# Kernel optimization log

Measured on AMD Instinct MI355X. Metric: run time of the kernel, lower is better.

## Reference

```python
import jax, jax.numpy as jnp
import numpy as np

S, B, H = 512, 64, 1024


def setup_inputs() -> dict:
    key = jax.random.key(0)
    ks = jax.random.split(key, 9)
    sc = 1.0 / np.sqrt(2 * H)
    return {
        "hidden": jax.random.normal(ks[0], (B, H), jnp.float32),
        "decoder_out": jax.random.normal(ks[1], (B, H), jnp.float32),
        "encoder_states": jax.random.normal(ks[2], (S, B, H), jnp.float32),
        "W_attn": jax.random.uniform(ks[3], (2 * H, 2 * H), jnp.float32, -sc, sc),
        "b_attn": jax.random.uniform(ks[4], (2 * H,), jnp.float32, -sc, sc),
        "W_attn2": jax.random.uniform(ks[5], (1, 2 * H), jnp.float32, -sc, sc),
        "b_attn2": jax.random.uniform(ks[6], (1,), jnp.float32, -sc, sc),
        "W_comb": jax.random.uniform(ks[7], (H, 2 * H), jnp.float32, -sc, sc),
        "b_comb": jax.random.uniform(ks[8], (H,), jnp.float32, -sc, sc),
    }


def reference(hidden, decoder_out, encoder_states, W_attn, b_attn, W_attn2, b_attn2, W_comb, b_comb):
    s, b, h = encoder_states.shape
    # per-timestep cat(hidden, enc_t) -> attn -> tanh -> attn2, fully batched over S
    hid = jnp.broadcast_to(hidden[None], (s, b, h))
    cat = jnp.concatenate([hid, encoder_states], axis=-1)            # [S,B,2H]
    scores = jnp.tanh(cat @ W_attn.T + b_attn) @ W_attn2.T + b_attn2  # [S,B,1]
    scores = scores[..., 0].T                                         # [B,S] (stack dim=1 + squeeze)
    attn_w = jax.nn.softmax(scores, axis=-1)                          # [B,S]
    # bmm([B,1,S], [B,S,H]) -> [B,H]
    applied = jnp.einsum("bs,sbh->bh", attn_w, encoder_states)
    out = jnp.concatenate([decoder_out, applied], axis=-1) @ W_comb.T + b_comb
    out = jnp.tanh(out)
    return out, applied
```

## Files before the change

### kernel.cpp

```cpp
#include <hip/hip_runtime.h>
#include <stdint.h>


typedef __attribute__((ext_vector_type(8))) short bf16x8;
typedef __attribute__((ext_vector_type(4))) float f32x4;

__device__ __forceinline__ float bf2f(uint16_t u) {
  return __uint_as_float(((uint32_t)u) << 16);
}
__device__ __forceinline__ uint16_t f2bf(float x) {
  uint32_t u = __float_as_uint(x);
  u += 0x7fffu + ((u >> 16) & 1u);
  return (uint16_t)(u >> 16);
}
__device__ __forceinline__ uint32_t pk2(float a, float b) {
  return (uint32_t)f2bf(a) | ((uint32_t)f2bf(b) << 16);
}
__device__ __forceinline__ uint4 cvt8(const float* __restrict__ p) {
  const float4 a = *(const float4*)p;
  const float4 b = *(const float4*)(p + 4);
  uint4 r;
  r.x = pk2(a.x, a.y); r.y = pk2(a.z, a.w);
  r.z = pk2(b.x, b.y); r.w = pk2(b.z, b.w);
  return r;
}
__device__ __forceinline__ float tanh_fast(float x) {
  const float e = __expf(2.f * x);
  return __builtin_fmaf(-2.f, __builtin_amdgcn_rcpf(e + 1.f), 1.f);
}
__device__ __forceinline__ void load16(const uint16_t* g, uint16_t* l) {
  __builtin_amdgcn_global_load_lds(
      (const __attribute__((address_space(1))) void*)g,
      (__attribute__((address_space(3))) void*)l, 16, 0, 0);
}

__global__ __launch_bounds__(256)
void cvt_all_kernel(const float* __restrict__ enc, const float* __restrict__ Wa,
                    const float* __restrict__ Wc,
                    uint16_t* __restrict__ enc_bf, uint16_t* __restrict__ Wa_bf,
                    uint16_t* __restrict__ Wc_bf,
                    float* __restrict__ scores, float* __restrict__ U,
                    const float* __restrict__ ba) {
  const int tid0 = blockIdx.x * 256 + threadIdx.x;
  if (tid0 < 32768) {
    scores[tid0] = 0.f;
#pragma unroll
    for (int k = 0; k < 4; ++k) {
      const int i = tid0 * 4 + k;
      U[i] = ba[i & 2047];
    }
  }
  const int stride = gridDim.x * 256;
  for (int idx = tid0; idx < 4718592; idx += stride) {
    if (idx < 4194304) {
      ((uint4*)enc_bf)[idx] = cvt8(enc + (size_t)idx * 8);
    } else if (idx < 4456448) {
      const int k = idx - 4194304;
      const int j = k >> 7, c8 = k & 127;
      ((uint4*)Wa_bf)[k] = cvt8(Wa + (size_t)j * 2048 + 1024 + c8 * 8);
    } else {
      const int k = idx - 4456448;
      ((uint4*)Wc_bf)[k] = cvt8(Wc + (size_t)k * 8);
    }
  }
}

__global__ __launch_bounds__(256)
void gemm_u_kernel(const float* __restrict__ A, const float* __restrict__ B32,
                   float* __restrict__ U) {
  __shared__ __align__(16) uint16_t sA[128 * 32];
  __shared__ __align__(16) uint16_t sB[128 * 32];
  const int t = threadIdx.x, lane = t & 63, wave = t >> 6;
  const int wm = wave >> 1, wn = wave & 1;
  const int bn0 = blockIdx.x * 128;
  const int kbase = blockIdx.y * 256;
  const int srow = t >> 2, scol = (t & 3) * 8;
  const int ar0 = min(srow, 63), ar1 = min(64 + srow, 63);
  f32x4 acc[4][4];
#pragma unroll
  for (int i = 0; i < 4; ++i)
#pragma unroll
    for (int j = 0; j < 4; ++j) acc[i][j] = (f32x4){0.f, 0.f, 0.f, 0.f};
  const int mrow = wm * 64 + (lane & 15);
  const int nrow = wn * 64 + (lane & 15);
  const int kq = (lane >> 4) * 8;
  for (int kk = 0; kk < 8; ++kk) {
    const int k0 = kbase + (kk << 5);
    const uint4 va0 = cvt8(A + (size_t)ar0 * 1024 + scol + k0);
    const uint4 va1 = cvt8(A + (size_t)ar1 * 1024 + scol + k0);
    const uint4 vb0 = cvt8(B32 + (size_t)(bn0 + srow) * 2048 + scol + k0);
    const uint4 vb1 = cvt8(B32 + (size_t)(bn0 + 64 + srow) * 2048 + scol + k0);
    __syncthreads();
    *(uint4*)&sA[t * 8] = va0;
    *(uint4*)&sA[2048 + t * 8] = va1;
    *(uint4*)&sB[t * 8] = vb0;
    *(uint4*)&sB[2048 + t * 8] = vb1;
    __syncthreads();
    bf16x8 af[4], bfr[4];
#pragma unroll
    for (int i = 0; i < 4; ++i) af[i] = *(const bf16x8*)&sA[(mrow + i * 16) * 32 + kq];
#pragma unroll
    for (int j = 0; j < 4; ++j) bfr[j] = *(const bf16x8*)&sB[(nrow + j * 16) * 32 + kq];
#pragma unroll
    for (int i = 0; i < 4; ++i)
#pragma unroll
      for (int j = 0; j < 4; ++j)
        acc[i][j] = __builtin_amdgcn_mfma_f32_16x16x32_bf16(af[i], bfr[j], acc[i][j], 0, 0, 0);
  }
  const int colb = lane & 15, rquad = lane >> 4;
#pragma unroll
  for (int i = 0; i < 4; ++i)
#pragma unroll
    for (int r = 0; r < 4; ++r) {
      const int gm = wm * 64 + i * 16 + rquad * 4 + r;
      if (gm < 64) {
#pragma unroll
        for (int j = 0; j < 4; ++j) {
          const int gn = bn0 + wn * 64 + j * 16 + colb;
          atomicAdd(&U[gm * 2048 + gn], acc[i][j][r]);
        }
      }
    }
}

__global__ __launch_bounds__(512, 2)
void gemm_score_kernel(const uint16_t* __restrict__ A,
                       const uint16_t* __restrict__ Bm,
                       float* __restrict__ outf,
                       const float* __restrict__ Ubias,
                       const float* __restrict__ bias) {
  __shared__ __align__(16) uint16_t lds[3][2][8192];

  const int t = threadIdx.x, lane = t & 63, wave = t >> 6;
  const int wm = wave >> 2, wn = wave & 3;
  const int wid = blockIdx.x;
  const int xcd = wid & 7, q = wid >> 3;
  const int bm0 = (xcd * 16 + (q >> 3)) * 256;
  const int bn0 = (q & 7) * 256;

  const uint16_t* gpA[2];
  const uint16_t* gpB[2];
  int sb[2];
#pragma unroll
  for (int qq = 0; qq < 2; ++qq) {
    const int s = qq * 512 + t;
    const int r = s >> 2, kc = s & 3;
    const int g = kc ^ ((r >> 1) & 3);
    gpA[qq] = A + (size_t)(bm0 + r) * 1024 + g * 8;
    gpB[qq] = Bm + (size_t)(bn0 + r) * 1024 + g * 8;
    sb[qq] = (qq * 512 + wave * 64) * 8;
  }

  f32x4 acc[8][4];
#pragma unroll
  for (int i = 0; i < 8; ++i)
#pragma unroll
    for (int j = 0; j < 4; ++j) acc[i][j] = (f32x4){0.f, 0.f, 0.f, 0.f};

  const int swz = ((lane >> 1) & 3) << 3;
  const int kq = ((lane >> 4) * 8) ^ swz;
  const int aoff = (wm * 128 + (lane & 15)) * 32 + kq;
  const int boff = (wn * 64 + (lane & 15)) * 32 + kq;

#pragma unroll
  for (int qq = 0; qq < 2; ++qq) {
    load16(gpA[qq], &lds[0][0][sb[qq]]);
    load16(gpB[qq], &lds[0][1][sb[qq]]);
  }
#pragma unroll
  for (int qq = 0; qq < 2; ++qq) {
    load16(gpA[qq] + 32, &lds[1][0][sb[qq]]);
    load16(gpB[qq] + 32, &lds[1][1][sb[qq]]);
  }
  asm volatile("s_waitcnt vmcnt(4)" ::: "memory");
  __builtin_amdgcn_s_barrier();

  constexpr int NT = 32;
#pragma unroll
  for (int kt = 0; kt < NT; ++kt) {
    const int bufc = kt % 3;
    if (kt + 2 < NT) {
      const int nb = (kt + 2) % 3;
      const int kpre = (kt + 2) * 32;
#pragma unroll
      for (int qq = 0; qq < 2; ++qq) {
        load16(gpA[qq] + kpre, &lds[nb][0][sb[qq]]);
        load16(gpB[qq] + kpre, &lds[nb][1][sb[qq]]);
      }
    }
    const uint16_t* sA = lds[bufc][0];
    const uint16_t* sB = lds[bufc][1];
    bf16x8 af[8], bfr[4];
#pragma unroll
    for (int i = 0; i < 8; ++i) af[i] = *(const bf16x8*)&sA[aoff + i * 512];
#pragma unroll
    for (int j = 0; j < 4; ++j) bfr[j] = *(const bf16x8*)&sB[boff + j * 512];
#pragma unroll
    for (int i = 0; i < 8; ++i)
#pragma unroll
      for (int j = 0; j < 4; ++j)
        acc[i][j] = __builtin_amdgcn_mfma_f32_16x16x32_bf16(af[i], bfr[j], acc[i][j], 0, 0, 0);
    if (kt + 2 < NT) {
      asm volatile("s_waitcnt vmcnt(4) lgkmcnt(0)" ::: "memory");
      __builtin_amdgcn_s_barrier();
    } else if (kt + 1 < NT) {
      asm volatile("s_waitcnt vmcnt(0) lgkmcnt(0)" ::: "memory");
      __builtin_amdgcn_s_barrier();
    }
  }

  const int colb = lane & 15, rquad = lane >> 4;
  float w2f[4];
#pragma unroll
  for (int j = 0; j < 4; ++j) w2f[j] = bias[bn0 + wn * 64 + j * 16 + colb];
#pragma unroll
  for (int i = 0; i < 8; ++i) {
#pragma unroll
    for (int r = 0; r < 4; ++r) {
      const int gm = bm0 + wm * 128 + i * 16 + rquad * 4 + r;
      const int bb = gm & 63;
      float p = 0.f;
#pragma unroll
      for (int j = 0; j < 4; ++j) {
        const float u = Ubias[bb * 2048 + bn0 + wn * 64 + j * 16 + colb];
        p += tanh_fast(acc[i][j][r] + u) * w2f[j];
      }
      p += __shfl_xor(p, 1);
      p += __shfl_xor(p, 2);
      p += __shfl_xor(p, 4);
      p += __shfl_xor(p, 8);
      if (colb == 0) atomicAdd(outf + gm, p);
    }
  }
}

template <int NT>
__global__ __launch_bounds__(256)
void gemm_comb_kernel(const uint16_t* __restrict__ A, int lda,
                      const uint16_t* __restrict__ Bm, int ldb,
                      int M, float* __restrict__ outf,
                      const float* __restrict__ bias) {
  __shared__ __align__(16) uint16_t lds[3][2][4096];

  const int t = threadIdx.x, lane = t & 63, wave = t >> 6;
  const int wm = wave >> 1, wn = wave & 1;
  const int bm0 = 0;
  const int bn0 = blockIdx.y * 128;
  const int kbase = blockIdx.z * (NT * 32);

  const uint16_t* gpA[2];
  const uint16_t* gpB[2];
  int sb[2];
#pragma unroll
  for (int q = 0; q < 2; ++q) {
    const int s = q * 256 + t;
    const int r = s >> 2, kc = s & 3;
    const int g = kc ^ ((r >> 1) & 3);
    gpA[q] = A + (size_t)min(bm0 + r, M - 1) * lda + kbase + g * 8;
    gpB[q] = Bm + (size_t)(bn0 + r) * ldb + kbase + g * 8;
    sb[q] = (q * 256 + wave * 64) * 8;
  }

  f32x4 acc[4][4];
#pragma unroll
  for (int i = 0; i < 4; ++i)
#pragma unroll
    for (int j = 0; j < 4; ++j) acc[i][j] = (f32x4){0.f, 0.f, 0.f, 0.f};

  const int swz = ((lane >> 1) & 3) << 3;
  const int kq = ((lane >> 4) * 8) ^ swz;
  const int aoff = (wm * 64 + (lane & 15)) * 32 + kq;
  const int boff = (wn * 64 + (lane & 15)) * 32 + kq;

#pragma unroll
  for (int q = 0; q < 2; ++q) {
    load16(gpA[q], &lds[0][0][sb[q]]);
    load16(gpB[q], &lds[0][1][sb[q]]);
  }
#pragma unroll
  for (int q = 0; q < 2; ++q) {
    load16(gpA[q] + 32, &lds[1][0][sb[q]]);
    load16(gpB[q] + 32, &lds[1][1][sb[q]]);
  }
  asm volatile("s_waitcnt vmcnt(4)" ::: "memory");
  __builtin_amdgcn_s_barrier();

#pragma unroll
  for (int kt = 0; kt < NT; ++kt) {
    const int bufc = kt % 3;
    if (kt + 2 < NT) {
      const int nb = (kt + 2) % 3;
      const int kpre = (kt + 2) * 32;
#pragma unroll
      for (int q = 0; q < 2; ++q) {
        load16(gpA[q] + kpre, &lds[nb][0][sb[q]]);
        load16(gpB[q] + kpre, &lds[nb][1][sb[q]]);
      }
    }
    const uint16_t* sA = lds[bufc][0];
    const uint16_t* sB = lds[bufc][1];
    bf16x8 af[4], bfr[4];
#pragma unroll
    for (int i = 0; i < 4; ++i) af[i] = *(const bf16x8*)&sA[aoff + i * 512];
#pragma unroll
    for (int j = 0; j < 4; ++j) bfr[j] = *(const bf16x8*)&sB[boff + j * 512];
#pragma unroll
    for (int i = 0; i < 4; ++i)
#pragma unroll
      for (int j = 0; j < 4; ++j)
        acc[i][j] = __builtin_amdgcn_mfma_f32_16x16x32_bf16(af[i], bfr[j], acc[i][j], 0, 0, 0);
    if (kt + 2 < NT) {
      asm volatile("s_waitcnt vmcnt(4) lgkmcnt(0)" ::: "memory");
      __builtin_amdgcn_s_barrier();
    } else if (kt + 1 < NT) {
      asm volatile("s_waitcnt vmcnt(0) lgkmcnt(0)" ::: "memory");
      __builtin_amdgcn_s_barrier();
    }
  }

  const int colb = lane & 15, rquad = lane >> 4;
  const float bsc = (blockIdx.z == 0) ? 1.f : 0.f;
#pragma unroll
  for (int i = 0; i < 4; ++i)
#pragma unroll
    for (int r = 0; r < 4; ++r) {
      const int gm = bm0 + wm * 64 + i * 16 + rquad * 4 + r;
      if (gm < M) {
#pragma unroll
        for (int j = 0; j < 4; ++j) {
          const int gn = bn0 + wn * 64 + j * 16 + colb;
          atomicAdd(outf + gm * 1024 + gn, acc[i][j][r] + bsc * bias[gn]);
        }
      }
    }
}

__global__ __launch_bounds__(256)
void applied_kernel(const uint16_t* __restrict__ encb, const float* __restrict__ dec,
                    const float* __restrict__ scores,
                    float* __restrict__ out_applied, uint16_t* __restrict__ acat,
                    float* __restrict__ out_acc) {
  const int b = blockIdx.x, chunk = blockIdx.y, t = threadIdx.x;
  const int wave = t >> 6, lane = t & 63;
  __shared__ float w[512];
  __shared__ float red[8];
  __shared__ float2 part2[256];
  float v0 = scores[(size_t)t * 64 + b];
  float v1 = scores[(size_t)(t + 256) * 64 + b];
  float mx = fmaxf(v0, v1);
#pragma unroll
  for (int off = 32; off >= 1; off >>= 1) mx = fmaxf(mx, __shfl_xor(mx, off));
  if (lane == 0) red[wave] = mx;
  __syncthreads();
  mx = fmaxf(fmaxf(red[0], red[1]), fmaxf(red[2], red[3]));
  const float e0 = __expf(v0 - mx), e1 = __expf(v1 - mx);
  float sum = e0 + e1;
#pragma unroll
  for (int off = 32; off >= 1; off >>= 1) sum += __shfl_xor(sum, off);
  if (lane == 0) red[4 + wave] = sum;
  __syncthreads();
  sum = (red[4] + red[5]) + (red[6] + red[7]);
  const float inv = 1.f / sum;
  w[t] = e0 * inv;
  w[t + 256] = e1 * inv;
  __syncthreads();
  const int hp = t & 31, sq = t >> 5;
  const int h = chunk * 64 + hp * 2;
  const uint32_t* base = (const uint32_t*)encb + (size_t)b * 512 + (h >> 1);
  float a0 = 0.f, a1 = 0.f;
#pragma unroll 8
  for (int s = sq * 64; s < sq * 64 + 64; ++s) {
    const uint32_t p = base[(size_t)s * 32768];
    a0 += w[s] * bf2f((uint16_t)(p & 0xffffu));
    a1 += w[s] * bf2f((uint16_t)(p >> 16));
  }
  part2[t] = make_float2(a0, a1);
  __syncthreads();
  if (t < 32) {
    a0 = 0.f; a1 = 0.f;
#pragma unroll
    for (int k = 0; k < 8; ++k) {
      const float2 pp = part2[t + 32 * k];
      a0 += pp.x; a1 += pp.y;
    }
    *(float2*)(out_applied + (size_t)b * 1024 + h) = make_float2(a0, a1);
    *(uint32_t*)(acat + (size_t)b * 2048 + 1024 + h) = pk2(a0, a1);
    *(uint32_t*)(acat + (size_t)b * 2048 + h) =
        pk2(dec[(size_t)b * 1024 + h], dec[(size_t)b * 1024 + h + 1]);
    *(float2*)(out_acc + (size_t)b * 1024 + h) = make_float2(0.f, 0.f);
  }
}

__global__ __launch_bounds__(256)
void tanh_kernel(const float* __restrict__ acc, float* __restrict__ outp) {
  const int i = blockIdx.x * 256 + threadIdx.x;
  float4 v = ((const float4*)acc)[i];
  v.x = tanh_fast(v.x); v.y = tanh_fast(v.y);
  v.z = tanh_fast(v.z); v.w = tanh_fast(v.w);
  ((float4*)outp)[i] = v;
}

extern "C" void kernel_launch(void* const* d_in, const int* in_sizes, int n_in,
                              void* d_out, int out_size, void* d_ws, size_t ws_size,
                              hipStream_t stream) {
  const float* hidden  = (const float*)d_in[0];
  const float* dec     = (const float*)d_in[1];
  const float* enc     = (const float*)d_in[2];
  const float* W_attn  = (const float*)d_in[3];
  const float* b_attn  = (const float*)d_in[4];
  const float* W_attn2 = (const float*)d_in[5];
  const float* W_comb  = (const float*)d_in[7];
  const float* b_comb  = (const float*)d_in[8];
  float* outp = (float*)d_out;

  char* ws = (char*)d_ws;
  float*    scores = (float*)(ws + 0);
  float*    U      = (float*)(ws + 131072);
  float*    out_acc= (float*)(ws + 131072);
  uint16_t* acat   = (uint16_t*)(ws + 655360);
  uint16_t* enc_bf = (uint16_t*)(ws + 1048576);
  uint16_t* Wa_bf  = (uint16_t*)(ws + 68157440);
  uint16_t* Wc_bf  = (uint16_t*)(ws + 72351744);

  cvt_all_kernel<<<4608, 256, 0, stream>>>(enc, W_attn, W_comb, enc_bf, Wa_bf,
                                           Wc_bf, scores, U, b_attn);
  gemm_u_kernel<<<dim3(16, 4), 256, 0, stream>>>(hidden, W_attn, U);
  gemm_score_kernel<<<1024, 512, 0, stream>>>(enc_bf, Wa_bf, scores, U, W_attn2);
  applied_kernel<<<dim3(64, 16), 256, 0, stream>>>(enc_bf, dec, scores,
                                                   outp + 65536, acat, out_acc);
  gemm_comb_kernel<16><<<dim3(1, 8, 4), 256, 0, stream>>>(
      acat, 2048, Wc_bf, 2048, 64, out_acc, b_comb);
  tanh_kernel<<<64, 256, 0, stream>>>(out_acc, outp);
}
```

Before: 451.8 us.

## Switch score GEMM to double-buffered K=64 tiles with 8-way XOR swizzle

```diff
diff --git a/kernel.cpp b/kernel.cpp
--- a/kernel.cpp
+++ b/kernel.cpp
@@ -129,7 +129,7 @@
                        float* __restrict__ outf,
                        const float* __restrict__ Ubias,
                        const float* __restrict__ bias) {
-  __shared__ __align__(16) uint16_t lds[3][2][8192];
+  __shared__ __align__(16) uint16_t lds[2][2][16384];
 
   const int t = threadIdx.x, lane = t & 63, wave = t >> 6;
   const int wm = wave >> 2, wn = wave & 3;
@@ -138,14 +138,14 @@
   const int bm0 = (xcd * 16 + (q >> 3)) * 256;
   const int bn0 = (q & 7) * 256;
 
-  const uint16_t* gpA[2];
-  const uint16_t* gpB[2];
-  int sb[2];
-#pragma unroll
-  for (int qq = 0; qq < 2; ++qq) {
+  const uint16_t* gpA[4];
+  const uint16_t* gpB[4];
+  int sb[4];
+#pragma unroll
+  for (int qq = 0; qq < 4; ++qq) {
     const int s = qq * 512 + t;
-    const int r = s >> 2, kc = s & 3;
-    const int g = kc ^ ((r >> 1) & 3);
+    const int r = s >> 3, kc = s & 7;
+    const int g = kc ^ (r & 7);
     gpA[qq] = A + (size_t)(bm0 + r) * 1024 + g * 8;
     gpB[qq] = Bm + (size_t)(bn0 + r) * 1024 + g * 8;
     sb[qq] = (qq * 512 + wave * 64) * 8;
@@ -157,54 +157,61 @@
 #pragma unroll
     for (int j = 0; j < 4; ++j) acc[i][j] = (f32x4){0.f, 0.f, 0.f, 0.f};
 
-  const int swz = ((lane >> 1) & 3) << 3;
-  const int kq = ((lane >> 4) * 8) ^ swz;
-  const int aoff = (wm * 128 + (lane & 15)) * 32 + kq;
-  const int boff = (wn * 64 + (lane & 15)) * 32 + kq;
-
-#pragma unroll
-  for (int qq = 0; qq < 2; ++qq) {
+  const int rl = lane & 15, kqh = lane >> 4, l7 = lane & 7;
+  const int cx0 = (kqh ^ l7) * 8;
+  const int cx1 = ((4 + kqh) ^ l7) * 8;
+  const int abase = (wm * 128 + rl) * 64;
+  const int bbase = (wn * 64 + rl) * 64;
+
+#pragma unroll
+  for (int qq = 0; qq < 4; ++qq) {
     load16(gpA[qq], &lds[0][0][sb[qq]]);
     load16(gpB[qq], &lds[0][1][sb[qq]]);
   }
-#pragma unroll
-  for (int qq = 0; qq < 2; ++qq) {
-    load16(gpA[qq] + 32, &lds[1][0][sb[qq]]);
-    load16(gpB[qq] + 32, &lds[1][1][sb[qq]]);
-  }
-  asm volatile("s_waitcnt vmcnt(4)" ::: "memory");
+  asm volatile("s_waitcnt vmcnt(0)" ::: "memory");
   __builtin_amdgcn_s_barrier();
 
-  constexpr int NT = 32;
+  constexpr int NT = 16;
 #pragma unroll
   for (int kt = 0; kt < NT; ++kt) {
-    const int bufc = kt % 3;
-    if (kt + 2 < NT) {
-      const int nb = (kt + 2) % 3;
-      const int kpre = (kt + 2) * 32;
-#pragma unroll
-      for (int qq = 0; qq < 2; ++qq) {
-        load16(gpA[qq] + kpre, &lds[nb][0][sb[qq]]);
-        load16(gpB[qq] + kpre, &lds[nb][1][sb[qq]]);
+    const int cb = kt & 1;
+    if (kt + 1 < NT) {
+      const int nb = cb ^ 1;
+      const int ko = (kt + 1) * 64;
+#pragma unroll
+      for (int qq = 0; qq < 4; ++qq) {
+        load16(gpA[qq] + ko, &lds[nb][0][sb[qq]]);
+        load16(gpB[qq] + ko, &lds[nb][1][sb[qq]]);
       }
     }
-    const uint16_t* sA = lds[bufc][0];
-    const uint16_t* sB = lds[bufc][1];
-    bf16x8 af[8], bfr[4];
-#pragma unroll
-    for (int i = 0; i < 8; ++i) af[i] = *(const bf16x8*)&sA[aoff + i * 512];
-#pragma unroll
-    for (int j = 0; j < 4; ++j) bfr[j] = *(const bf16x8*)&sB[boff + j * 512];
-#pragma unroll
-    for (int i = 0; i < 8; ++i)
-#pragma unroll
-      for (int j = 0; j < 4; ++j)
-        acc[i][j] = __builtin_amdgcn_mfma_f32_16x16x32_bf16(af[i], bfr[j], acc[i][j], 0, 0, 0);
-    if (kt + 2 < NT) {
-      asm volatile("s_waitcnt vmcnt(4) lgkmcnt(0)" ::: "memory");
-      __builtin_amdgcn_s_barrier();
-    } else if (kt + 1 < NT) {
-      asm volatile("s_waitcnt vmcnt(0) lgkmcnt(0)" ::: "memory");
+    const uint16_t* sA = lds[cb][0];
+    const uint16_t* sB = lds[cb][1];
+    {
+      bf16x8 af[8], bfr[4];
+#pragma unroll
+      for (int i = 0; i < 8; ++i) af[i] = *(const bf16x8*)&sA[abase + i * 1024 + cx0];
+#pragma unroll
+      for (int j = 0; j < 4; ++j) bfr[j] = *(const bf16x8*)&sB[bbase + j * 1024 + cx0];
+#pragma unroll
+      for (int i = 0; i < 8; ++i)
+#pragma unroll
+        for (int j = 0; j < 4; ++j)
+          acc[i][j] = __builtin_amdgcn_mfma_f32_16x16x32_bf16(af[i], bfr[j], acc[i][j], 0, 0, 0);
+    }
+    {
+      bf16x8 af[8], bfr[4];
+#pragma unroll
+      for (int i = 0; i < 8; ++i) af[i] = *(const bf16x8*)&sA[abase + i * 1024 + cx1];
+#pragma unroll
+      for (int j = 0; j < 4; ++j) bfr[j] = *(const bf16x8*)&sB[bbase + j * 1024 + cx1];
+#pragma unroll
+      for (int i = 0; i < 8; ++i)
+#pragma unroll
+        for (int j = 0; j < 4; ++j)
+          acc[i][j] = __builtin_amdgcn_mfma_f32_16x16x32_bf16(af[i], bfr[j], acc[i][j], 0, 0, 0);
+    }
+    if (kt + 1 < NT) {
+      asm volatile("s_waitcnt vmcnt(0)" ::: "memory");
       __builtin_amdgcn_s_barrier();
     }
   }
```

Result: no change. 444.3 us (-1.7%).

## Split score GEMM k-step into two phases with interleaved loads and MFMA priority

Applied to the files above, without the earlier changes.

```diff
diff --git a/kernel.cpp b/kernel.cpp
--- a/kernel.cpp
+++ b/kernel.cpp
@@ -129,7 +129,7 @@
                        float* __restrict__ outf,
                        const float* __restrict__ Ubias,
                        const float* __restrict__ bias) {
-  __shared__ __align__(16) uint16_t lds[3][2][8192];
+  __shared__ __align__(16) uint16_t lds[4][2][8192];
 
   const int t = threadIdx.x, lane = t & 63, wave = t >> 6;
   const int wm = wave >> 2, wn = wave & 3;
@@ -143,8 +143,8 @@
   int sb[2];
 #pragma unroll
   for (int qq = 0; qq < 2; ++qq) {
-    const int s = qq * 512 + t;
-    const int r = s >> 2, kc = s & 3;
+    const int sl = qq * 512 + t;
+    const int r = sl >> 2, kc = sl & 3;
     const int g = kc ^ ((r >> 1) & 3);
     gpA[qq] = A + (size_t)(bm0 + r) * 1024 + g * 8;
     gpB[qq] = Bm + (size_t)(bn0 + r) * 1024 + g * 8;
@@ -159,52 +159,70 @@
 
   const int swz = ((lane >> 1) & 3) << 3;
   const int kq = ((lane >> 4) * 8) ^ swz;
-  const int aoff = (wm * 128 + (lane & 15)) * 32 + kq;
-  const int boff = (wn * 64 + (lane & 15)) * 32 + kq;
-
-#pragma unroll
-  for (int qq = 0; qq < 2; ++qq) {
-    load16(gpA[qq], &lds[0][0][sb[qq]]);
-    load16(gpB[qq], &lds[0][1][sb[qq]]);
-  }
-#pragma unroll
-  for (int qq = 0; qq < 2; ++qq) {
-    load16(gpA[qq] + 32, &lds[1][0][sb[qq]]);
-    load16(gpB[qq] + 32, &lds[1][1][sb[qq]]);
-  }
+  const int rl = lane & 15;
+  const int aoff = (wm * 128 + rl) * 32 + kq;
+  const int boff = (wn * 64 + rl) * 32 + kq;
+
+#pragma unroll
+  for (int qq = 0; qq < 2; ++qq) load16(gpA[qq], &lds[0][0][sb[qq]]);
+#pragma unroll
+  for (int qq = 0; qq < 2; ++qq) load16(gpB[qq], &lds[0][1][sb[qq]]);
+#pragma unroll
+  for (int qq = 0; qq < 2; ++qq) load16(gpA[qq] + 32, &lds[1][0][sb[qq]]);
+#pragma unroll
+  for (int qq = 0; qq < 2; ++qq) load16(gpB[qq] + 32, &lds[1][1][sb[qq]]);
   asm volatile("s_waitcnt vmcnt(4)" ::: "memory");
   __builtin_amdgcn_s_barrier();
 
-  constexpr int NT = 32;
-#pragma unroll
-  for (int kt = 0; kt < NT; ++kt) {
-    const int bufc = kt % 3;
-    if (kt + 2 < NT) {
-      const int nb = (kt + 2) % 3;
-      const int kpre = (kt + 2) * 32;
-#pragma unroll
-      for (int qq = 0; qq < 2; ++qq) {
-        load16(gpA[qq] + kpre, &lds[nb][0][sb[qq]]);
-        load16(gpB[qq] + kpre, &lds[nb][1][sb[qq]]);
-      }
-    }
-    const uint16_t* sA = lds[bufc][0];
-    const uint16_t* sB = lds[bufc][1];
+  constexpr int NS = 32;
+#pragma unroll
+  for (int s = 0; s < NS; ++s) {
+    const int cb = s & 3;
+    const uint16_t* sA = lds[cb][0];
+    const uint16_t* sB = lds[cb][1];
     bf16x8 af[8], bfr[4];
-#pragma unroll
-    for (int i = 0; i < 8; ++i) af[i] = *(const bf16x8*)&sA[aoff + i * 512];
+    if (s + 2 < NS) {
+      const int nb = (s + 2) & 3, ko = (s + 2) * 32;
+#pragma unroll
+      for (int qq = 0; qq < 2; ++qq) load16(gpA[qq] + ko, &lds[nb][0][sb[qq]]);
+    }
+#pragma unroll
+    for (int i = 0; i < 4; ++i) af[i] = *(const bf16x8*)&sA[aoff + i * 512];
 #pragma unroll
     for (int j = 0; j < 4; ++j) bfr[j] = *(const bf16x8*)&sB[boff + j * 512];
-#pragma unroll
-    for (int i = 0; i < 8; ++i)
+    __builtin_amdgcn_s_barrier();
+    asm volatile("s_waitcnt lgkmcnt(0)" ::: "memory");
+    __builtin_amdgcn_sched_barrier(0);
+    __builtin_amdgcn_s_setprio(1);
+#pragma unroll
+    for (int i = 0; i < 4; ++i)
 #pragma unroll
       for (int j = 0; j < 4; ++j)
         acc[i][j] = __builtin_amdgcn_mfma_f32_16x16x32_bf16(af[i], bfr[j], acc[i][j], 0, 0, 0);
-    if (kt + 2 < NT) {
-      asm volatile("s_waitcnt vmcnt(4) lgkmcnt(0)" ::: "memory");
+    __builtin_amdgcn_s_setprio(0);
+    __builtin_amdgcn_s_barrier();
+    if (s + 2 < NS) {
+      const int nb = (s + 2) & 3, ko = (s + 2) * 32;
+#pragma unroll
+      for (int qq = 0; qq < 2; ++qq) load16(gpB[qq] + ko, &lds[nb][1][sb[qq]]);
+    }
+#pragma unroll
+    for (int i = 4; i < 8; ++i) af[i] = *(const bf16x8*)&sA[aoff + i * 512];
+    __builtin_amdgcn_s_barrier();
+    asm volatile("s_waitcnt lgkmcnt(0)" ::: "memory");
+    __builtin_amdgcn_sched_barrier(0);
+    __builtin_amdgcn_s_setprio(1);
+#pragma unroll
+    for (int i = 4; i < 8; ++i)
+#pragma unroll
+      for (int j = 0; j < 4; ++j)
+        acc[i][j] = __builtin_amdgcn_mfma_f32_16x16x32_bf16(af[i], bfr[j], acc[i][j], 0, 0, 0);
+    __builtin_amdgcn_s_setprio(0);
+    if (s < 30) {
+      asm volatile("s_waitcnt vmcnt(4)" ::: "memory");
       __builtin_amdgcn_s_barrier();
-    } else if (kt + 1 < NT) {
-      asm volatile("s_waitcnt vmcnt(0) lgkmcnt(0)" ::: "memory");
+    } else if (s == 30) {
+      asm volatile("s_waitcnt vmcnt(0)" ::: "memory");
       __builtin_amdgcn_s_barrier();
     }
   }
```

Measured after the change: 455.8 us. About the same (+0.9%).
